# Optimization experiments

Measured on AMD Instinct MI355X. Metric: run time of the kernel, lower is better.

## Reference

```python
import jax, jax.numpy as jnp
import numpy as np

B, S, D, H = 2, 2048, 2048, 16
HD = D // H
FF = 4 * D
EPS = 1e-5
SCALE = 1.0 / np.sqrt(D)  # source uses 1/sqrt(d_out), not 1/sqrt(head_dim)


def _gelu_tanh(x):
    c = np.sqrt(2.0 / np.pi).astype(np.float32)
    return 0.5 * x * (1.0 + jnp.tanh(c * (x + 0.044715 * x * x * x)))


def _layernorm(x, scale, shift):
    mean = jnp.mean(x, axis=-1, keepdims=True)
    var = jnp.mean(jnp.square(x - mean), axis=-1, keepdims=True)  # correction=0
    return (x - mean) * jax.lax.rsqrt(var + EPS) * scale + shift


def setup_inputs() -> dict:
    key = jax.random.key(0)
    ks = jax.random.split(key, 10)
    init = lambda k, shape, fan_in: (jax.random.normal(k, shape, jnp.float32) / np.sqrt(fan_in))
    return {
        "x": jax.random.normal(ks[0], (B, S, D), jnp.float32),
        "wq": init(ks[1], (D, D), D),
        "wk": init(ks[2], (D, D), D),
        "wv": init(ks[3], (D, D), D),
        "wo": init(ks[4], (D, D), D),
        "bo": jnp.zeros((D,), jnp.float32),
        "g1": jnp.ones((D,), jnp.float32),
        "s1": jnp.zeros((D,), jnp.float32),
        "g2": jnp.ones((D,), jnp.float32),
        "s2": jnp.zeros((D,), jnp.float32),
        "w1": init(ks[5], (D, FF), D),
        "b1": jnp.zeros((FF,), jnp.float32),
        "w2": init(ks[6], (FF, D), FF),
        "b2": jnp.zeros((D,), jnp.float32),
    }


def _block(x, wq, wk, wv, wo, bo, g1, s1, g2, s2, w1, b1, w2, b2):
    # pre-LN attention
    h = _layernorm(x, g1, s1)
    q = (h @ wq).reshape(B, S, H, HD).transpose(0, 2, 1, 3)  # [B,H,S,HD]
    k = (h @ wk).reshape(B, S, H, HD).transpose(0, 2, 1, 3)
    v = (h @ wv).reshape(B, S, H, HD).transpose(0, 2, 1, 3)
    scores = jnp.einsum('bhqd,bhkd->bhqk', q, k) * SCALE
    causal = jnp.tril(jnp.ones((S, S), dtype=bool))  # mask strictly-upper
    scores = jnp.where(causal, scores, -jnp.inf)
    attn = jax.nn.softmax(scores, axis=-1)
    ctx = jnp.einsum('bhqk,bhkd->bhqd', attn, v)
    ctx = ctx.transpose(0, 2, 1, 3).reshape(B, S, D)
    x = x + ctx @ wo + bo
    # pre-LN FFN
    h = _layernorm(x, g2, s2)
    h = _gelu_tanh(h @ w1 + b1) @ w2 + b2
    return x + h


def reference(x, wq, wk, wv, wo, bo, g1, s1, g2, s2, w1, b1, w2, b2):
    return _block(x, wq, wk, wv, wo, bo, g1, s1, g2, s2, w1, b1, w2, b2)
```

## Files before the change

kernel.cpp:

```cpp
#include <hip/hip_runtime.h>
#include <hip/hip_bf16.h>
#include <cstdint>

constexpr float SCALE_QK = 0.02209708691207961f;
constexpr float LOG2E    = 1.4426950408889634f;

using short8 = __attribute__((ext_vector_type(8))) short;
using f32x4  = __attribute__((ext_vector_type(4))) float;
using ushort4v = __attribute__((ext_vector_type(4))) ushort;

#define MFMA16(a,b,c) __builtin_amdgcn_mfma_f32_16x16x32_bf16((a),(b),(c),0,0,0)

__device__ __forceinline__ ushort f2bf(float f){
  uint32_t u = __builtin_bit_cast(uint32_t, f);
  u += 0x7fffu + ((u >> 16) & 1u);
  return (ushort)(u >> 16);
}

__device__ __forceinline__ void gload_lds16(const void* g, void* l){
  __builtin_amdgcn_global_load_lds(
      (const __attribute__((address_space(1))) void*)g,
      (__attribute__((address_space(3))) void*)l, 16, 0, 0);
}

__global__ __launch_bounds__(256) void ln_kernel(
    const float* __restrict__ x, const float* __restrict__ g,
    const float* __restrict__ sh, ushort* __restrict__ out){
  const int row = blockIdx.x, t = threadIdx.x;
  const float* xr = x + (size_t)row*2048 + t*8;
  float v[8];
  *(float4*)&v[0] = *(const float4*)(xr);
  *(float4*)&v[4] = *(const float4*)(xr + 4);
  float s = 0.f, sq = 0.f;
#pragma unroll
  for (int i = 0; i < 8; ++i){ s += v[i]; sq += v[i]*v[i]; }
#pragma unroll
  for (int d = 1; d < 64; d <<= 1){ s += __shfl_xor(s, d, 64); sq += __shfl_xor(sq, d, 64); }
  __shared__ float red[8];
  const int w = t >> 6, lane = t & 63;
  if (lane == 0){ red[w] = s; red[4 + w] = sq; }
  __syncthreads();
  s  = red[0] + red[1] + red[2] + red[3];
  sq = red[4] + red[5] + red[6] + red[7];
  const float mean = s * (1.f/2048.f);
  const float inv  = rsqrtf(sq * (1.f/2048.f) - mean*mean + 1e-5f);
  union { ushort u[8]; uint4 v4; } o;
#pragma unroll
  for (int i = 0; i < 8; ++i){
    int j = t*8 + i;
    o.u[i] = f2bf((v[i] - mean) * inv * g[j] + sh[j]);
  }
  *(uint4*)(out + (size_t)row*2048 + t*8) = o.v4;
}

__global__ __launch_bounds__(256) void wconv_t(
    const float* __restrict__ in, ushort* __restrict__ out, int K, int N){
  __shared__ ushort tile[32][34];
  const int tx = threadIdx.x & 31, ty = threadIdx.x >> 5;
  const int n0 = blockIdx.x * 32, k0 = blockIdx.y * 32;
#pragma unroll
  for (int r = 0; r < 4; ++r){
    int kk = ty + r*8;
    tile[kk][tx] = f2bf(in[(size_t)(k0 + kk)*N + n0 + tx]);
  }
  __syncthreads();
#pragma unroll
  for (int r = 0; r < 4; ++r){
    int nn = ty + r*8;
    out[(size_t)(n0 + nn)*K + k0 + tx] = tile[tx][nn];
  }
}

__global__ __launch_bounds__(256) void wconv4(
    const float* __restrict__ w0, const float* __restrict__ w1p,
    const float* __restrict__ w2p, const float* __restrict__ w3p,
    ushort* __restrict__ out){
  __shared__ ushort tile[32][34];
  const int tx = threadIdx.x & 31, ty = threadIdx.x >> 5;
  const int n0 = blockIdx.x * 32, k0 = blockIdx.y * 32, z = blockIdx.z;
  const float* in = (z == 0) ? w0 : (z == 1) ? w1p : (z == 2) ? w2p : w3p;
  ushort* o = out + (size_t)z * 4194304;
#pragma unroll
  for (int r = 0; r < 4; ++r){
    int kk = ty + r*8;
    tile[kk][tx] = f2bf(in[(size_t)(k0 + kk)*2048 + n0 + tx]);
  }
  __syncthreads();
#pragma unroll
  for (int r = 0; r < 4; ++r){
    int nn = ty + r*8;
    o[(size_t)(n0 + nn)*2048 + k0 + tx] = tile[tx][nn];
  }
}

template<int EPI>
__global__ __launch_bounds__(256) void gemm_bt(
    const ushort* __restrict__ A, const ushort* __restrict__ Bt,
    int N, int K, void* __restrict__ outp,
    const float* __restrict__ resid, const float* __restrict__ bias){
  __shared__ ushort lds[2][128*64];
  const int tid = threadIdx.x, lane = tid & 63, wid = tid >> 6;
  const int wr = wid >> 1, wc = wid & 1;
  const int l15 = lane & 15, l4 = lane >> 4;

  const int bid = blockIdx.x;
  const int xcd = bid & 7, j = bid >> 3;
  const int mb = xcd*4 + (j & 3);
  const int nb = j >> 2;
  const int m0 = mb * 128, n0 = nb * 128;

  f32x4 acc[4][4];
#pragma unroll
  for (int mi = 0; mi < 4; ++mi)
#pragma unroll
    for (int ni = 0; ni < 4; ++ni) acc[mi][ni] = (f32x4){0.f,0.f,0.f,0.f};

  const ushort* Abase = A  + (size_t)m0*K;
  const ushort* Bbase = Bt + (size_t)n0*K;

  const int NTk = K >> 6;
  for (int kt = 0; kt < NTk; ++kt){
    if (kt) __syncthreads();
#pragma unroll
    for (int i = 0; i < 4; ++i){
      const int chunk = (i*4 + wid)*64 + lane;
      const int row = chunk >> 3;
      const int c8  = (chunk & 7) ^ (row & 7);
      const size_t goff = (size_t)row*K + (size_t)kt*64 + c8*8;
      gload_lds16(Abase + goff, (ushort*)&lds[0][0] + (size_t)(i*4 + wid)*512);
      gload_lds16(Bbase + goff, (ushort*)&lds[1][0] + (size_t)(i*4 + wid)*512);
    }
    __syncthreads();

#pragma unroll
    for (int kk = 0; kk < 2; ++kk){
      short8 af[4], bf[4];
      const int kb = kk*4 + l4;
#pragma unroll
      for (int i = 0; i < 4; ++i){
        const int rA = wr*64 + i*16 + l15;
        af[i] = *(const short8*)&lds[0][rA*64 + ((kb ^ (rA & 7))*8)];
        const int rB = wc*64 + i*16 + l15;
        bf[i] = *(const short8*)&lds[1][rB*64 + ((kb ^ (rB & 7))*8)];
      }
#pragma unroll
      for (int mi = 0; mi < 4; ++mi)
#pragma unroll
        for (int ni = 0; ni < 4; ++ni)
          acc[mi][ni] = MFMA16(af[mi], bf[ni], acc[mi][ni]);
    }
  }

  if constexpr (EPI == 0){
    __syncthreads();
    ushort* tile = (ushort*)&lds[0][0];
    const int which = n0 >> 11;
    const int hh = (n0 & 2047) >> 7;
    const int bb = m0 >> 11, srow0 = m0 & 2047;
    if (which != 2){
      const float qs = (which == 0) ? SCALE_QK * LOG2E : 1.0f;
#pragma unroll
      for (int mi = 0; mi < 4; ++mi)
#pragma unroll
        for (int ni = 0; ni < 4; ++ni){
          const int rl = wr*64 + mi*16 + l4*4;
          const int cl = wc*64 + ni*16 + l15;
#pragma unroll
          for (int j2 = 0; j2 < 4; ++j2)
            tile[(rl + j2)*128 + cl] = f2bf(acc[mi][ni][j2] * qs);
        }
      __syncthreads();
      ushort* dst = (ushort*)outp + (size_t)which*8388608 +
                    ((size_t)(bb*16 + hh)*2048 + srow0)*128;
#pragma unroll
      for (int i = 0; i < 8; ++i){
        const int c = i*256 + tid, row = c >> 4, d8 = (c & 15)*8;
        *(uint4*)(dst + (size_t)row*128 + d8) = *(const uint4*)&tile[row*128 + d8];
      }
    } else {
#pragma unroll
      for (int mi = 0; mi < 4; ++mi)
#pragma unroll
        for (int ni = 0; ni < 4; ++ni){
          const int rl = wr*64 + mi*16 + l4*4;
          const int cl = wc*64 + ni*16 + l15;
          ushort4v o;
#pragma unroll
          for (int j2 = 0; j2 < 4; ++j2) o[j2] = f2bf(acc[mi][ni][j2]);
          *(ushort4v*)&tile[cl*128 + rl] = o;
        }
      __syncthreads();
      ushort* dst = (ushort*)outp + (size_t)2*8388608 +
                    (size_t)(bb*16 + hh)*262144 + srow0;
#pragma unroll
      for (int i = 0; i < 8; ++i){
        const int c = i*256 + tid, drow = c >> 4, s8 = (c & 15)*8;
        *(uint4*)(dst + (size_t)drow*2048 + s8) = *(const uint4*)&tile[drow*128 + s8];
      }
    }
  } else {
#pragma unroll
    for (int mi = 0; mi < 4; ++mi){
#pragma unroll
      for (int ni = 0; ni < 4; ++ni){
        const int rloc = wr*64 + mi*16 + l4*4;
        const int col  = n0 + wc*64 + ni*16 + l15;
#pragma unroll
        for (int j2 = 0; j2 < 4; ++j2){
          const int m = m0 + rloc + j2;
          float v = acc[mi][ni][j2];
          if constexpr (EPI == 1){
            ((float*)outp)[(size_t)m*N + col] = resid[(size_t)m*N + col] + bias[col] + v;
          } else {
            const float xx = v + bias[col];
            const float z  = 0.7978845608f*(xx + 0.044715f*xx*xx*xx);
            const float t  = __expf(-2.f*fabsf(z));
            const float th = (1.f - t)/(1.f + t);
            const float gl = 0.5f*xx*(1.f + copysignf(th, xx));
            ((ushort*)outp)[(size_t)m*N + col] = f2bf(gl);
          }
        }
      }
    }
  }
}

__global__ __launch_bounds__(256, 2) void attn_kernel(
    const ushort* __restrict__ q, const ushort* __restrict__ k,
    const ushort* __restrict__ vt, ushort* __restrict__ ctx){
  __shared__ ushort k_lds[2][64*128];
  __shared__ ushort v_lds[2][128*64];
  __shared__ ushort p_lds[4][32*64];
  const int tid = threadIdx.x, lane = tid & 63, w = tid >> 6;
  const int l15 = lane & 15, l4 = lane >> 4;
  const int id = blockIdx.x;
  const int bh = id & 31;
  const int r  = id >> 5;
  const int qt = (r < 8) ? (15 - r) : (r - 8);
  const int bb = bh >> 4, hh = bh & 15;
  const ushort* kbase = k  + (size_t)bh * 262144;
  const ushort* vbase = vt + (size_t)bh * 262144;

  short8 qf[2][4];
#pragma unroll
  for (int mi = 0; mi < 2; ++mi){
    const int s = qt*128 + w*32 + mi*16 + l15;
    const ushort* qr = q + ((size_t)bh*2048 + s)*128 + l4*8;
#pragma unroll
    for (int kk = 0; kk < 4; ++kk) qf[mi][kk] = *(const short8*)(qr + kk*32);
  }

  f32x4 cacc[2][8];
#pragma unroll
  for (int mi = 0; mi < 2; ++mi)
#pragma unroll
    for (int dt = 0; dt < 8; ++dt) cacc[mi][dt] = (f32x4){0.f,0.f,0.f,0.f};
  float mrun[2][4], lrun[2][4];
#pragma unroll
  for (int mi = 0; mi < 2; ++mi)
#pragma unroll
    for (int j = 0; j < 4; ++j){ mrun[mi][j] = -1e30f; lrun[mi][j] = 0.f; }

  auto stage = [&](int buf, int t){
    const ushort* ksrc = kbase + (size_t)t*8192;
#pragma unroll
    for (int i = 0; i < 4; ++i){
      const int base = i*256 + w*64;
      const int chunk = base + lane;
      const int kr = chunk >> 4;
      const int c8 = (chunk & 15) ^ (kr & 7);
      gload_lds16(ksrc + (size_t)kr*128 + c8*8, &k_lds[buf][(size_t)base*8]);
    }
#pragma unroll
    for (int i = 0; i < 4; ++i){
      const int base = i*256 + w*64;
      const int chunk = base + lane;
      const int vr = chunk >> 3;
      const int c8 = (chunk & 7) ^ (vr & 7);
      gload_lds16(vbase + (size_t)vr*2048 + t*64 + c8*8, &v_lds[buf][(size_t)base*8]);
    }
  };

  const int nt = 2*qt + 2;
  stage(0, 0);
  __syncthreads();
  int cur = 0;
  for (int t = 0; t < nt; ++t){
    if (t + 1 < nt) stage(cur ^ 1, t + 1);

    const bool skip = (t == 2*qt + 1) && (w < 2);
    if (!skip){
      f32x4 sa[2][4];
#pragma unroll
      for (int mi = 0; mi < 2; ++mi)
#pragma unroll
        for (int ct = 0; ct < 4; ++ct) sa[mi][ct] = (f32x4){0.f,0.f,0.f,0.f};
      __builtin_amdgcn_s_setprio(1);
#pragma unroll
      for (int kk = 0; kk < 4; ++kk){
#pragma unroll
        for (int ct = 0; ct < 4; ++ct){
          const int kr = ct*16 + l15;
          short8 kf = *(const short8*)&k_lds[cur][kr*128 + (((kk*4 + l4) ^ (kr & 7))*8)];
          sa[0][ct] = MFMA16(qf[0][kk], kf, sa[0][ct]);
          sa[1][ct] = MFMA16(qf[1][kk], kf, sa[1][ct]);
        }
      }
      __builtin_amdgcn_s_setprio(0);

      const bool anymask = (t >= 2*qt) && !((t == 2*qt) && (w >= 2));
      float rowlm[2][4];
      bool over = false;
#pragma unroll
      for (int mi = 0; mi < 2; ++mi){
#pragma unroll
        for (int j = 0; j < 4; ++j){
          const int qa = qt*128 + w*32 + mi*16 + l4*4 + j;
          float lm = -1e30f;
#pragma unroll
          for (int ct = 0; ct < 4; ++ct){
            float sc = sa[mi][ct][j];
            if (anymask){
              const int ka = t*64 + ct*16 + l15;
              sc = (ka > qa) ? -1e30f : sc;
            }
            sa[mi][ct][j] = sc;
            lm = fmaxf(lm, sc);
          }
          rowlm[mi][j] = lm;
          over = over || (lm > mrun[mi][j] + 8.f);
        }
      }
      if (__any(over)){
#pragma unroll
        for (int mi = 0; mi < 2; ++mi)
#pragma unroll
          for (int j = 0; j < 4; ++j){
            float mx = rowlm[mi][j];
#pragma unroll
            for (int d = 1; d < 16; d <<= 1) mx = fmaxf(mx, __shfl_xor(mx, d, 16));
            const float mnew = fmaxf(mrun[mi][j], mx);
            const float corr = exp2f(mrun[mi][j] - mnew);
            mrun[mi][j] = mnew; lrun[mi][j] *= corr;
#pragma unroll
            for (int dt = 0; dt < 8; ++dt) cacc[mi][dt][j] *= corr;
          }
      }
#pragma unroll
      for (int mi = 0; mi < 2; ++mi)
#pragma unroll
        for (int j = 0; j < 4; ++j){
          float psum = 0.f;
#pragma unroll
          for (int ct = 0; ct < 4; ++ct){
            const float p = exp2f(sa[mi][ct][j] - mrun[mi][j]);
            sa[mi][ct][j] = p; psum += p;
          }
          lrun[mi][j] += psum;
        }

#pragma unroll
      for (int mi = 0; mi < 2; ++mi)
#pragma unroll
        for (int ct = 0; ct < 4; ++ct)
#pragma unroll
          for (int j = 0; j < 4; ++j){
            const int row = mi*16 + l4*4 + j, col = ct*16 + l15;
            p_lds[w][row*64 + ((col >> 3) ^ (row & 7))*8 + (col & 7)] = f2bf(sa[mi][ct][j]);
          }

      __builtin_amdgcn_s_setprio(1);
#pragma unroll
      for (int kk2 = 0; kk2 < 2; ++kk2){
        const int kb = kk2*4 + l4;
        short8 pa0 = *(const short8*)&p_lds[w][l15*64 + ((kb ^ (l15 & 7))*8)];
        short8 pa1 = *(const short8*)&p_lds[w][(16 + l15)*64 + ((kb ^ (l15 & 7))*8)];
#pragma unroll
        for (int dt = 0; dt < 8; ++dt){
          const int vr = dt*16 + l15;
          short8 vf = *(const short8*)&v_lds[cur][vr*64 + ((kb ^ (vr & 7))*8)];
          cacc[0][dt] = MFMA16(pa0, vf, cacc[0][dt]);
          cacc[1][dt] = MFMA16(pa1, vf, cacc[1][dt]);
        }
      }
      __builtin_amdgcn_s_setprio(0);
    }

    if (t + 1 < nt){ __syncthreads(); cur ^= 1; }
  }

#pragma unroll
  for (int mi = 0; mi < 2; ++mi){
    float inv[4];
#pragma unroll
    for (int j = 0; j < 4; ++j){
      float lt = lrun[mi][j];
#pragma unroll
      for (int d = 1; d < 16; d <<= 1) lt += __shfl_xor(lt, d, 16);
      inv[j] = 1.f / lt;
    }
#pragma unroll
    for (int dt = 0; dt < 8; ++dt)
#pragma unroll
      for (int j = 0; j < 4; ++j){
        const int s = qt*128 + w*32 + mi*16 + l4*4 + j;
        const int d = dt*16 + l15;
        ctx[((size_t)(bb*2048 + s))*2048 + hh*128 + d] = f2bf(cacc[mi][dt][j] * inv[j]);
      }
  }
}

extern "C" void kernel_launch(void* const* d_in, const int* in_sizes, int n_in,
                              void* d_out, int out_size, void* d_ws, size_t ws_size,
                              hipStream_t stream) {
  const float* x  = (const float*)d_in[0];
  const float* wq = (const float*)d_in[1];
  const float* wk = (const float*)d_in[2];
  const float* wv = (const float*)d_in[3];
  const float* wo = (const float*)d_in[4];
  const float* bo = (const float*)d_in[5];
  const float* g1 = (const float*)d_in[6];
  const float* s1 = (const float*)d_in[7];
  const float* g2 = (const float*)d_in[8];
  const float* s2 = (const float*)d_in[9];
  const float* w1 = (const float*)d_in[10];
  const float* b1 = (const float*)d_in[11];
  const float* w2 = (const float*)d_in[12];
  const float* b2 = (const float*)d_in[13];
  float* out = (float*)d_out;
  char* ws = (char*)d_ws;

  ushort* wqkvT = (ushort*)(ws + 0);
  ushort* woT = (ushort*)(ws + 25165824);
  ushort* w1T = (ushort*)(ws + 33554432);
  ushort* w2T = (ushort*)(ws + 67108864);
  ushort* h1  = (ushort*)(ws + 100663296);
  ushort* qb  = (ushort*)(ws + 117440512);
  ushort* kb  = (ushort*)(ws + 134217728);
  ushort* vtb = (ushort*)(ws + 150994944);
  ushort* ctxb= (ushort*)(ws + 184549376);
  float*  x2  = (float*)(ws + 201326592);
  ushort* h2  = (ushort*)(ws + 234881024);
  ushort* ffb = (ushort*)(ws + 117440512);

  wconv4<<<dim3(64, 64, 4), 256, 0, stream>>>(wq, wk, wv, wo, wqkvT);
  wconv_t<<<dim3(256, 64), 256, 0, stream>>>(w1, w1T, 2048, 8192);
  wconv_t<<<dim3(64, 256), 256, 0, stream>>>(w2, w2T, 8192, 2048);

  ln_kernel<<<4096, 256, 0, stream>>>(x, g1, s1, h1);

  gemm_bt<0><<<32*48, 256, 0, stream>>>(h1, wqkvT, 6144, 2048, qb, nullptr, nullptr);

  attn_kernel<<<512, 256, 0, stream>>>(qb, kb, vtb, ctxb);

  gemm_bt<1><<<32*16, 256, 0, stream>>>(ctxb, woT, 2048, 2048, x2, x, bo);

  ln_kernel<<<4096, 256, 0, stream>>>(x2, g2, s2, h2);

  gemm_bt<2><<<32*64, 256, 0, stream>>>(h2, w1T, 8192, 2048, ffb, nullptr, b1);
  gemm_bt<1><<<32*16, 256, 0, stream>>>(ffb, w2T, 2048, 8192, out, x2, b2);

  (void)in_sizes; (void)n_in; (void)out_size; (void)ws_size;
}
```

Measured before the change: 673.0 us.

## Use 8 waves per attention block with 16 query rows each; merge FFN weight conversions

The attention kernel now runs 512 threads per block, so each of 8 waves owns 16 query rows instead of 32. The K/V staging loads, causal skip/mask conditions and the P scratch buffer are reworked to match. This halves per-wave accumulator registers and adds waves per block to hide latency, at the cost of each wave reading more K/V from LDS per MFMA. The two FFN weight transpose-convert launches are also merged into one 3D-grid kernel to drop a launch.

```diff
diff --git a/kernel.cpp b/kernel.cpp
--- a/kernel.cpp
+++ b/kernel.cpp
@@ -53,24 +53,6 @@
   *(uint4*)(out + (size_t)row*2048 + t*8) = o.v4;
 }
 
-__global__ __launch_bounds__(256) void wconv_t(
-    const float* __restrict__ in, ushort* __restrict__ out, int K, int N){
-  __shared__ ushort tile[32][34];
-  const int tx = threadIdx.x & 31, ty = threadIdx.x >> 5;
-  const int n0 = blockIdx.x * 32, k0 = blockIdx.y * 32;
-#pragma unroll
-  for (int r = 0; r < 4; ++r){
-    int kk = ty + r*8;
-    tile[kk][tx] = f2bf(in[(size_t)(k0 + kk)*N + n0 + tx]);
-  }
-  __syncthreads();
-#pragma unroll
-  for (int r = 0; r < 4; ++r){
-    int nn = ty + r*8;
-    out[(size_t)(n0 + nn)*K + k0 + tx] = tile[tx][nn];
-  }
-}
-
 __global__ __launch_bounds__(256) void wconv4(
     const float* __restrict__ w0, const float* __restrict__ w1p,
     const float* __restrict__ w2p, const float* __restrict__ w3p,
@@ -90,6 +72,30 @@
   for (int r = 0; r < 4; ++r){
     int nn = ty + r*8;
     o[(size_t)(n0 + nn)*2048 + k0 + tx] = tile[tx][nn];
+  }
+}
+
+__global__ __launch_bounds__(256) void wconv_ffn(
+    const float* __restrict__ w1, const float* __restrict__ w2,
+    ushort* __restrict__ w1T, ushort* __restrict__ w2T){
+  __shared__ ushort tile[32][34];
+  const int tx = threadIdx.x & 31, ty = threadIdx.x >> 5;
+  const int z = blockIdx.z;
+  const float* in; ushort* out; int K, N, n0, k0;
+  if (z == 0){ in = w1; out = w1T; K = 2048; N = 8192;
+               n0 = blockIdx.x * 32; k0 = blockIdx.y * 32; }
+  else       { in = w2; out = w2T; K = 8192; N = 2048;
+               n0 = blockIdx.y * 32; k0 = blockIdx.x * 32; }
+#pragma unroll
+  for (int r = 0; r < 4; ++r){
+    int kk = ty + r*8;
+    tile[kk][tx] = f2bf(in[(size_t)(k0 + kk)*N + n0 + tx]);
+  }
+  __syncthreads();
+#pragma unroll
+  for (int r = 0; r < 4; ++r){
+    int nn = ty + r*8;
+    out[(size_t)(n0 + nn)*K + k0 + tx] = tile[tx][nn];
   }
 }
 
@@ -225,12 +231,12 @@
   }
 }
 
-__global__ __launch_bounds__(256, 2) void attn_kernel(
+__global__ __launch_bounds__(512, 2) void attn_kernel(
     const ushort* __restrict__ q, const ushort* __restrict__ k,
     const ushort* __restrict__ vt, ushort* __restrict__ ctx){
   __shared__ ushort k_lds[2][64*128];
   __shared__ ushort v_lds[2][128*64];
-  __shared__ ushort p_lds[4][32*64];
+  __shared__ ushort p_lds[8][16*64];
   const int tid = threadIdx.x, lane = tid & 63, w = tid >> 6;
   const int l15 = lane & 15, l4 = lane >> 4;
   const int id = blockIdx.x;
@@ -241,39 +247,34 @@
   const ushort* kbase = k  + (size_t)bh * 262144;
   const ushort* vbase = vt + (size_t)bh * 262144;
 
-  short8 qf[2][4];
-#pragma unroll
-  for (int mi = 0; mi < 2; ++mi){
-    const int s = qt*128 + w*32 + mi*16 + l15;
+  short8 qf[4];
+  {
+    const int s = qt*128 + w*16 + l15;
     const ushort* qr = q + ((size_t)bh*2048 + s)*128 + l4*8;
 #pragma unroll
-    for (int kk = 0; kk < 4; ++kk) qf[mi][kk] = *(const short8*)(qr + kk*32);
-  }
-
-  f32x4 cacc[2][8];
-#pragma unroll
-  for (int mi = 0; mi < 2; ++mi)
-#pragma unroll
-    for (int dt = 0; dt < 8; ++dt) cacc[mi][dt] = (f32x4){0.f,0.f,0.f,0.f};
-  float mrun[2][4], lrun[2][4];
-#pragma unroll
-  for (int mi = 0; mi < 2; ++mi)
-#pragma unroll
-    for (int j = 0; j < 4; ++j){ mrun[mi][j] = -1e30f; lrun[mi][j] = 0.f; }
+    for (int kk = 0; kk < 4; ++kk) qf[kk] = *(const short8*)(qr + kk*32);
+  }
+
+  f32x4 cacc[8];
+#pragma unroll
+  for (int dt = 0; dt < 8; ++dt) cacc[dt] = (f32x4){0.f,0.f,0.f,0.f};
+  float mrun[4], lrun[4];
+#pragma unroll
+  for (int j = 0; j < 4; ++j){ mrun[j] = -1e30f; lrun[j] = 0.f; }
 
   auto stage = [&](int buf, int t){
     const ushort* ksrc = kbase + (size_t)t*8192;
 #pragma unroll
-    for (int i = 0; i < 4; ++i){
-      const int base = i*256 + w*64;
+    for (int i = 0; i < 2; ++i){
+      const int base = i*512 + w*64;
       const int chunk = base + lane;
       const int kr = chunk >> 4;
       const int c8 = (chunk & 15) ^ (kr & 7);
       gload_lds16(ksrc + (size_t)kr*128 + c8*8, &k_lds[buf][(size_t)base*8]);
     }
 #pragma unroll
-    for (int i = 0; i < 4; ++i){
-      const int base = i*256 + w*64;
+    for (int i = 0; i < 2; ++i){
+      const int base = i*512 + w*64;
       const int chunk = base + lane;
       const int vr = chunk >> 3;
       const int c8 = (chunk & 7) ^ (vr & 7);
@@ -288,13 +289,11 @@
   for (int t = 0; t < nt; ++t){
     if (t + 1 < nt) stage(cur ^ 1, t + 1);
 
-    const bool skip = (t == 2*qt + 1) && (w < 2);
+    const bool skip = (t == 2*qt + 1) && (w < 4);
     if (!skip){
-      f32x4 sa[2][4];
-#pragma unroll
-      for (int mi = 0; mi < 2; ++mi)
-#pragma unroll
-        for (int ct = 0; ct < 4; ++ct) sa[mi][ct] = (f32x4){0.f,0.f,0.f,0.f};
+      f32x4 sa[4];
+#pragma unroll
+      for (int ct = 0; ct < 4; ++ct) sa[ct] = (f32x4){0.f,0.f,0.f,0.f};
       __builtin_amdgcn_s_setprio(1);
 #pragma unroll
       for (int kk = 0; kk < 4; ++kk){
@@ -302,85 +301,73 @@
         for (int ct = 0; ct < 4; ++ct){
           const int kr = ct*16 + l15;
           short8 kf = *(const short8*)&k_lds[cur][kr*128 + (((kk*4 + l4) ^ (kr & 7))*8)];
-          sa[0][ct] = MFMA16(qf[0][kk], kf, sa[0][ct]);
-          sa[1][ct] = MFMA16(qf[1][kk], kf, sa[1][ct]);
+          sa[ct] = MFMA16(qf[kk], kf, sa[ct]);
         }
       }
       __builtin_amdgcn_s_setprio(0);
 
-      const bool anymask = (t >= 2*qt) && !((t == 2*qt) && (w >= 2));
-      float rowlm[2][4];
+      const bool anymask = (t >= 2*qt) && !((t == 2*qt) && (w >= 4));
+      float rowlm[4];
       bool over = false;
 #pragma unroll
-      for (int mi = 0; mi < 2; ++mi){
+      for (int j = 0; j < 4; ++j){
+        const int qa = qt*128 + w*16 + l4*4 + j;
+        float lm = -1e30f;
+#pragma unroll
+        for (int ct = 0; ct < 4; ++ct){
+          float sc = sa[ct][j];
+          if (anymask){
+            const int ka = t*64 + ct*16 + l15;
+            sc = (ka > qa) ? -1e30f : sc;
+          }
+          sa[ct][j] = sc;
+          lm = fmaxf(lm, sc);
+        }
+        rowlm[j] = lm;
+        over = over || (lm > mrun[j] + 8.f);
+      }
+      if (__any(over)){
 #pragma unroll
         for (int j = 0; j < 4; ++j){
-          const int qa = qt*128 + w*32 + mi*16 + l4*4 + j;
-          float lm = -1e30f;
-#pragma unroll
-          for (int ct = 0; ct < 4; ++ct){
-            float sc = sa[mi][ct][j];
-            if (anymask){
-              const int ka = t*64 + ct*16 + l15;
-              sc = (ka > qa) ? -1e30f : sc;
-            }
-            sa[mi][ct][j] = sc;
-            lm = fmaxf(lm, sc);
-          }
-          rowlm[mi][j] = lm;
-          over = over || (lm > mrun[mi][j] + 8.f);
-        }
-      }
-      if (__any(over)){
-#pragma unroll
-        for (int mi = 0; mi < 2; ++mi)
-#pragma unroll
-          for (int j = 0; j < 4; ++j){
-            float mx = rowlm[mi][j];
-#pragma unroll
-            for (int d = 1; d < 16; d <<= 1) mx = fmaxf(mx, __shfl_xor(mx, d, 16));
-            const float mnew = fmaxf(mrun[mi][j], mx);
-            const float corr = exp2f(mrun[mi][j] - mnew);
-            mrun[mi][j] = mnew; lrun[mi][j] *= corr;
-#pragma unroll
-            for (int dt = 0; dt < 8; ++dt) cacc[mi][dt][j] *= corr;
-          }
-      }
-#pragma unroll
-      for (int mi = 0; mi < 2; ++mi)
+          float mx = rowlm[j];
+#pragma unroll
+          for (int d = 1; d < 16; d <<= 1) mx = fmaxf(mx, __shfl_xor(mx, d, 16));
+          const float mnew = fmaxf(mrun[j], mx);
+          const float corr = exp2f(mrun[j] - mnew);
+          mrun[j] = mnew; lrun[j] *= corr;
+#pragma unroll
+          for (int dt = 0; dt < 8; ++dt) cacc[dt][j] *= corr;
+        }
+      }
+#pragma unroll
+      for (int j = 0; j < 4; ++j){
+        float psum = 0.f;
+#pragma unroll
+        for (int ct = 0; ct < 4; ++ct){
+          const float p = exp2f(sa[ct][j] - mrun[j]);
+          sa[ct][j] = p; psum += p;
+        }
+        lrun[j] += psum;
+      }
+
+#pragma unroll
+      for (int ct = 0; ct < 4; ++ct)
 #pragma unroll
         for (int j = 0; j < 4; ++j){
-          float psum = 0.f;
-#pragma unroll
-          for (int ct = 0; ct < 4; ++ct){
-            const float p = exp2f(sa[mi][ct][j] - mrun[mi][j]);
-            sa[mi][ct][j] = p; psum += p;
-          }
-          lrun[mi][j] += psum;
-        }
-
-#pragma unroll
-      for (int mi = 0; mi < 2; ++mi)
-#pragma unroll
-        for (int ct = 0; ct < 4; ++ct)
-#pragma unroll
-          for (int j = 0; j < 4; ++j){
-            const int row = mi*16 + l4*4 + j, col = ct*16 + l15;
-            p_lds[w][row*64 + ((col >> 3) ^ (row & 7))*8 + (col & 7)] = f2bf(sa[mi][ct][j]);
-          }
+          const int row = l4*4 + j, col = ct*16 + l15;
+          p_lds[w][row*64 + ((col >> 3) ^ (row & 7))*8 + (col & 7)] = f2bf(sa[ct][j]);
+        }
 
       __builtin_amdgcn_s_setprio(1);
 #pragma unroll
       for (int kk2 = 0; kk2 < 2; ++kk2){
         const int kb = kk2*4 + l4;
-        short8 pa0 = *(const short8*)&p_lds[w][l15*64 + ((kb ^ (l15 & 7))*8)];
-        short8 pa1 = *(const short8*)&p_lds[w][(16 + l15)*64 + ((kb ^ (l15 & 7))*8)];
+        short8 pa = *(const short8*)&p_lds[w][l15*64 + ((kb ^ (l15 & 7))*8)];
 #pragma unroll
         for (int dt = 0; dt < 8; ++dt){
           const int vr = dt*16 + l15;
           short8 vf = *(const short8*)&v_lds[cur][vr*64 + ((kb ^ (vr & 7))*8)];
-          cacc[0][dt] = MFMA16(pa0, vf, cacc[0][dt]);
-          cacc[1][dt] = MFMA16(pa1, vf, cacc[1][dt]);
+          cacc[dt] = MFMA16(pa, vf, cacc[dt]);
         }
       }
       __builtin_amdgcn_s_setprio(0);
@@ -389,25 +376,22 @@
     if (t + 1 < nt){ __syncthreads(); cur ^= 1; }
   }
 
-#pragma unroll
-  for (int mi = 0; mi < 2; ++mi){
-    float inv[4];
+  float inv[4];
+#pragma unroll
+  for (int j = 0; j < 4; ++j){
+    float lt = lrun[j];
+#pragma unroll
+    for (int d = 1; d < 16; d <<= 1) lt += __shfl_xor(lt, d, 16);
+    inv[j] = 1.f / lt;
+  }
+#pragma unroll
+  for (int dt = 0; dt < 8; ++dt)
 #pragma unroll
     for (int j = 0; j < 4; ++j){
-      float lt = lrun[mi][j];
-#pragma unroll
-      for (int d = 1; d < 16; d <<= 1) lt += __shfl_xor(lt, d, 16);
-      inv[j] = 1.f / lt;
-    }
-#pragma unroll
-    for (int dt = 0; dt < 8; ++dt)
-#pragma unroll
-      for (int j = 0; j < 4; ++j){
-        const int s = qt*128 + w*32 + mi*16 + l4*4 + j;
-        const int d = dt*16 + l15;
-        ctx[((size_t)(bb*2048 + s))*2048 + hh*128 + d] = f2bf(cacc[mi][dt][j] * inv[j]);
-      }
-  }
+      const int s = qt*128 + w*16 + l4*4 + j;
+      const int d = dt*16 + l15;
+      ctx[((size_t)(bb*2048 + s))*2048 + hh*128 + d] = f2bf(cacc[dt][j] * inv[j]);
+    }
 }
 
 extern "C" void kernel_launch(void* const* d_in, const int* in_sizes, int n_in,
@@ -444,14 +428,13 @@
   ushort* ffb = (ushort*)(ws + 117440512);
 
   wconv4<<<dim3(64, 64, 4), 256, 0, stream>>>(wq, wk, wv, wo, wqkvT);
-  wconv_t<<<dim3(256, 64), 256, 0, stream>>>(w1, w1T, 2048, 8192);
-  wconv_t<<<dim3(64, 256), 256, 0, stream>>>(w2, w2T, 8192, 2048);
+  wconv_ffn<<<dim3(256, 64, 2), 256, 0, stream>>>(w1, w2, w1T, w2T);
 
   ln_kernel<<<4096, 256, 0, stream>>>(x, g1, s1, h1);
 
   gemm_bt<0><<<32*48, 256, 0, stream>>>(h1, wqkvT, 6144, 2048, qb, nullptr, nullptr);
 
-  attn_kernel<<<512, 256, 0, stream>>>(qb, kb, vtb, ctxb);
+  attn_kernel<<<512, 512, 0, stream>>>(qb, kb, vtb, ctxb);
 
   gemm_bt<1><<<32*16, 256, 0, stream>>>(ctxb, woT, 2048, 2048, x2, x, bo);
 
```

Measured after the change: 676.3 us. No clear change (+0.5%).
